# Optimization experiments

Hardware: AMD Instinct MI355X
Metric: run time of the kernel (lower is better)

The kernel has to match this reference:

```python
import jax, jax.numpy as jnp
import numpy as np

# FlowNetC correlation hyperparameters (init_kwargs)
PAD = 4            # pad_size
KERNEL = 1         # kernel_size (1x1 patch)
MD = 4             # max_displacement
STRIDE1 = 1        # stride over output positions
STRIDE2 = 1        # stride over displacements


def setup_inputs() -> dict:
    key = jax.random.key(0)
    k1, k2 = jax.random.split(key)
    input1 = jax.random.normal(k1, (8, 256, 96, 128), dtype=jnp.float32)
    input2 = jax.random.normal(k2, (8, 256, 96, 128), dtype=jnp.float32)
    return {"input1": input1, "input2": input2}


def reference(input1, input2):
    # Cost volume: out[b, d, y, x] = (1/C) * sum_c input1[b,c,y,x] * input2[b,c,y+dy,x+dx]
    # for all displacements (dy, dx) in [-MD, MD] with step STRIDE2.
    # With pad_size == max_displacement, kernel_size == 1, stride1 == 1 the output
    # spatial grid equals the input grid (FlowNetC configuration). Normalization
    # matches correlation_cuda: sumelems = kernel_size^2 * C.
    B, C, H, W = input1.shape
    p2 = jnp.pad(input2, ((0, 0), (0, 0), (PAD, PAD), (PAD, PAD)))
    disp = range(-MD, MD + 1, STRIDE2)  # 9 offsets -> 81 displacement channels
    outs = []
    for dy in disp:
        for dx in disp:
            shifted = jax.lax.dynamic_slice(p2, (0, 0, PAD + dy, PAD + dx), (B, C, H, W))
            # mean over channels == sum / (KERNEL*KERNEL*C) since KERNEL == 1
            outs.append(jnp.mean(input1 * shifted, axis=1))
    return jnp.stack(outs, axis=1)  # [B, 81, H, W]
```

## Files before the change

### kernel.cpp

```cpp
#include <hip/hip_runtime.h>
#include <hip/hip_bf16.h>


#define B_ 8
#define C_ 256
#define H_ 96
#define W_ 128
#define HW_ 12288
#define CHW_ 3145728

#define BUFSZ 40960
#define IN1_OFF 0
#define IN2_OFF 8192
#define IN2_ROWB (32 * 64)

typedef __attribute__((ext_vector_type(8))) short short8;
typedef __attribute__((ext_vector_type(4))) float f32x4;

__device__ __forceinline__ int swz16(int g, int slot) {
    return (g ^ (slot & 3) ^ ((slot >> 2) & 3)) * 16;
}

__global__ __launch_bounds__(512, 2) void corr_mfma6(
    const float* __restrict__ in1,
    const float* __restrict__ in2,
    float* __restrict__ out)
{
    __shared__ __align__(16) char lds[2 * BUFSZ];

    const int tid = threadIdx.x;

    const int blk  = blockIdx.x;
    const int b    = blk & 7;
    const int rest = blk >> 3;
    const int yt   = rest >> 3;
    const int xh   = rest & 7;

    #pragma unroll
    for (int k = 0; k < 10; ++k)
        *(f32x4*)(lds + tid * 16 + k * 8192) = f32x4{0.f, 0.f, 0.f, 0.f};

    const int lane = tid & 63;
    const int wv   = tid >> 6;
    const int ut   = wv & 1;
    const int yrh  = wv >> 1;
    const int ln   = lane & 15;
    const int qd   = lane >> 4;

    const int offA0 = IN1_OFF + ((2 * yrh) * 16 + ln) * 64 + swz16(qd, ln);
    const int pB    = 16 * ut + ln;
    const int offB  = IN2_OFF + ((2 * yrh) * 32 + pB) * 64 + swz16(qd, pB);

    const float* in1b = in1 + (size_t)b * CHW_;
    const float* in2b = in2 + (size_t)b * CHW_;

    const int pp2 = tid & 7;
    const int g2  = (tid >> 3) & 3;
    const int r2i = tid >> 5;
    const int px2 = 4 * pp2;
    const int gx2 = xh * 16 - 8 + px2;
    const int ry2 = yt * 8 - 4 + r2i;
    const bool valid2 = (gx2 >= 0) && (gx2 <= 124) && (ry2 >= 0) && (ry2 < H_);
    const int slot2 = r2i * 32 + px2;
    const float* sp2base = in2b + (size_t)(8 * g2) * HW_ + ry2 * W_ + gx2;

    const int pq1 = tid & 3;
    const int jj1 = (tid >> 2) & 3;
    const int g1  = (tid >> 4) & 3;
    const int r1i = tid >> 6;
    const int px1 = 4 * pq1;
    const int gx1 = xh * 16 + px1;
    const int y1  = yt * 8 + r1i;
    const int slot1 = r1i * 16 + px1;
    const float* sp1base = in1b + (size_t)(8 * g1 + 2 * jj1) * HW_ + y1 * W_ + gx1;

    f32x4 rA2[8], rA1[2];
    f32x4 rB2[8], rB1[2];

    auto issueA = [&](int kc) {
        const size_t ch = (size_t)kc * 32 * HW_;
        if (valid2) {
            #pragma unroll
            for (int j = 0; j < 8; ++j)
                rA2[j] = *(const f32x4*)(sp2base + ch + (size_t)j * HW_);
        }
        rA1[0] = *(const f32x4*)(sp1base + ch);
        rA1[1] = *(const f32x4*)(sp1base + ch + HW_);
    };
    auto issueB = [&](int kc) {
        const size_t ch = (size_t)kc * 32 * HW_;
        if (valid2) {
            #pragma unroll
            for (int j = 0; j < 8; ++j)
                rB2[j] = *(const f32x4*)(sp2base + ch + (size_t)j * HW_);
        }
        rB1[0] = *(const f32x4*)(sp1base + ch);
        rB1[1] = *(const f32x4*)(sp1base + ch + HW_);
    };

    auto storeA = [&](char* __restrict__ buf) {
        if (valid2) {
            #pragma unroll
            for (int p = 0; p < 4; ++p) {
                union { __hip_bfloat162 h2[4]; short8 s8; } u;
                #pragma unroll
                for (int jj = 0; jj < 4; ++jj)
                    u.h2[jj] = __float22bfloat162_rn(float2{rA2[2 * jj][p], rA2[2 * jj + 1][p]});
                *(short8*)(buf + IN2_OFF + (slot2 + p) * 64 + swz16(g2, slot2 + p)) = u.s8;
            }
        }
        #pragma unroll
        for (int p = 0; p < 4; ++p) {
            __hip_bfloat162 h = __float22bfloat162_rn(float2{rA1[0][p], rA1[1][p]});
            *(__hip_bfloat162*)(buf + IN1_OFF + (slot1 + p) * 64 + swz16(g1, slot1 + p) + 4 * jj1) = h;
        }
    };
    auto storeB = [&](char* __restrict__ buf) {
        if (valid2) {
            #pragma unroll
            for (int p = 0; p < 4; ++p) {
                union { __hip_bfloat162 h2[4]; short8 s8; } u;
                #pragma unroll
                for (int jj = 0; jj < 4; ++jj)
                    u.h2[jj] = __float22bfloat162_rn(float2{rB2[2 * jj][p], rB2[2 * jj + 1][p]});
                *(short8*)(buf + IN2_OFF + (slot2 + p) * 64 + swz16(g2, slot2 + p)) = u.s8;
            }
        }
        #pragma unroll
        for (int p = 0; p < 4; ++p) {
            __hip_bfloat162 h = __float22bfloat162_rn(float2{rB1[0][p], rB1[1][p]});
            *(__hip_bfloat162*)(buf + IN1_OFF + (slot1 + p) * 64 + swz16(g1, slot1 + p) + 4 * jj1) = h;
        }
    };

    f32x4 acc0[9], acc1[9];
    #pragma unroll
    for (int s = 0; s < 9; ++s) { acc0[s] = f32x4{0.f,0.f,0.f,0.f}; acc1[s] = f32x4{0.f,0.f,0.f,0.f}; }

    auto compute = [&](const char* __restrict__ buf) {
        short8 a0  = *(const short8*)(buf + offA0);
        short8 a1  = *(const short8*)(buf + offA0 + 16 * 64);
        short8 blo = *(const short8*)(buf + offB);
        #pragma unroll
        for (int s = 0; s < 9; ++s) {
            short8 bhi = *(const short8*)(buf + offB + (s + 1) * IN2_ROWB);
            acc0[s] = __builtin_amdgcn_mfma_f32_16x16x32_bf16(a0, blo, acc0[s], 0, 0, 0);
            acc1[s] = __builtin_amdgcn_mfma_f32_16x16x32_bf16(a1, bhi, acc1[s], 0, 0, 0);
            blo = bhi;
        }
    };

    __syncthreads();

    issueA(0);
    issueB(1);

    #pragma unroll
    for (int k2 = 0; k2 < 4; ++k2) {
        storeA(lds);
        if (2 * k2 + 2 < 8) issueA(2 * k2 + 2);
        asm volatile("s_waitcnt lgkmcnt(0)" ::: "memory");
        __builtin_amdgcn_s_barrier();
        asm volatile("" ::: "memory");
        compute(lds);
        storeB(lds + BUFSZ);
        if (2 * k2 + 3 < 8) issueB(2 * k2 + 3);
        asm volatile("s_waitcnt lgkmcnt(0)" ::: "memory");
        __builtin_amdgcn_s_barrier();
        asm volatile("" ::: "memory");
        compute(lds + BUFSZ);
    }

    __syncthreads();

    const float scale = 1.0f / 256.0f;
    float* outb = out + (size_t)b * 81 * HW_ + (size_t)(yt * 8) * W_ + xh * 16;

    #pragma unroll
    for (int s = 0; s < 9; ++s) {
        #pragma unroll
        for (int yr = 0; yr < 2; ++yr) {
            const f32x4 a = yr ? acc1[s] : acc0[s];
            const int y = 2 * yrh + yr;
            #pragma unroll
            for (int r = 0; r < 4; ++r) {
                const int m  = qd * 4 + r;
                const int dx = ln - m - 8 + 16 * ut;
                if (dx >= -4 && dx <= 4)
                    *(float*)(lds + ((y * 9 + dx + 4) * 16 + m) * 4) = a[r] * scale;
            }
        }
        asm volatile("s_waitcnt lgkmcnt(0)" ::: "memory");
        __builtin_amdgcn_s_barrier();
        asm volatile("" ::: "memory");
        #pragma unroll
        for (int i = 0; i < 3; ++i) {
            const int pidx = i * 4 + qd;
            if (pidx < 9) {
                const float v = *(const float*)(lds + ((wv * 9 + pidx) * 16 + ln) * 4);
                outb[((size_t)(s * 9 + pidx) * H_ + wv) * W_ + ln] = v;
            }
        }
        asm volatile("s_waitcnt lgkmcnt(0)" ::: "memory");
        __builtin_amdgcn_s_barrier();
        asm volatile("" ::: "memory");
    }
}

extern "C" void kernel_launch(void* const* d_in, const int* in_sizes, int n_in,
                              void* d_out, int out_size, void* d_ws, size_t ws_size,
                              hipStream_t stream) {
    const float* in1 = (const float*)d_in[0];
    const float* in2 = (const float*)d_in[1];
    float* out = (float*)d_out;

    corr_mfma6<<<768, 512, 0, stream>>>(in1, in2, out);
}
```

Measured before the change: 245.7 us.

## Split displacement rows across three blocks and unify load roles

Each block now handles only three of the nine vertical displacement rows, so the grid grows threefold and each block loads a smaller in2 halo (10 rows instead of 16). The LDS buffers shrink and launch bounds allow four blocks per CU, which raises occupancy and cuts accumulator registers. Thread roles are reorganized so some threads load in2 rows and others load in1 rows, each with full 8-channel vector loads, in place of the earlier mixed per-thread scheme. The cost is that in1 tiles and overlapping in2 halo rows are now read by three blocks instead of one, which adds global/L2 traffic.

```diff
diff --git a/kernel.cpp b/kernel.cpp
--- a/kernel.cpp
+++ b/kernel.cpp
@@ -9,7 +9,7 @@
 #define HW_ 12288
 #define CHW_ 3145728
 
-#define BUFSZ 40960
+#define BUFSZ 28672
 #define IN1_OFF 0
 #define IN2_OFF 8192
 #define IN2_ROWB (32 * 64)
@@ -21,7 +21,7 @@
     return (g ^ (slot & 3) ^ ((slot >> 2) & 3)) * 16;
 }
 
-__global__ __launch_bounds__(512, 2) void corr_mfma6(
+__global__ __launch_bounds__(512, 4) void corr_mfma8(
     const float* __restrict__ in1,
     const float* __restrict__ in2,
     float* __restrict__ out)
@@ -33,11 +33,13 @@
     const int blk  = blockIdx.x;
     const int b    = blk & 7;
     const int rest = blk >> 3;
-    const int yt   = rest >> 3;
-    const int xh   = rest & 7;
+    const int dg   = rest % 3;
+    const int t    = rest / 3;
+    const int yt   = t >> 3;
+    const int xh   = t & 7;
 
     #pragma unroll
-    for (int k = 0; k < 10; ++k)
+    for (int k = 0; k < 7; ++k)
         *(f32x4*)(lds + tid * 16 + k * 8192) = f32x4{0.f, 0.f, 0.f, 0.f};
 
     const int lane = tid & 63;
@@ -54,95 +56,71 @@
     const float* in1b = in1 + (size_t)b * CHW_;
     const float* in2b = in2 + (size_t)b * CHW_;
 
-    const int pp2 = tid & 7;
-    const int g2  = (tid >> 3) & 3;
-    const int r2i = tid >> 5;
-    const int px2 = 4 * pp2;
-    const int gx2 = xh * 16 - 8 + px2;
-    const int ry2 = yt * 8 - 4 + r2i;
-    const bool valid2 = (gx2 >= 0) && (gx2 <= 124) && (ry2 >= 0) && (ry2 < H_);
-    const int slot2 = r2i * 32 + px2;
-    const float* sp2base = in2b + (size_t)(8 * g2) * HW_ + ry2 * W_ + gx2;
+    const bool isB = tid < 320;
+    const int r_   = isB ? (tid >> 5) : ((tid - 320) >> 4);
+    const int pxq  = isB ? ((tid >> 2) & 7) : ((tid >> 2) & 3);
+    const int g_   = tid & 3;
+    const int gx   = isB ? (xh * 16 - 8 + 4 * pxq) : (xh * 16 + 4 * pxq);
+    const int gy   = isB ? (yt * 8 - 4 + 3 * dg + r_) : (yt * 8 + r_);
+    const bool vld = isB ? (gx >= 0 && gx <= 124 && gy >= 0 && gy < H_)
+                         : (tid < 448);
+    const int slot = isB ? (r_ * 32 + 4 * pxq) : (r_ * 16 + 4 * pxq);
+    const int goff = isB ? IN2_OFF : IN1_OFF;
+    const float* spbase = (isB ? in2b : in1b) + (size_t)(8 * g_) * HW_ + gy * W_ + gx;
 
-    const int pq1 = tid & 3;
-    const int jj1 = (tid >> 2) & 3;
-    const int g1  = (tid >> 4) & 3;
-    const int r1i = tid >> 6;
-    const int px1 = 4 * pq1;
-    const int gx1 = xh * 16 + px1;
-    const int y1  = yt * 8 + r1i;
-    const int slot1 = r1i * 16 + px1;
-    const float* sp1base = in1b + (size_t)(8 * g1 + 2 * jj1) * HW_ + y1 * W_ + gx1;
-
-    f32x4 rA2[8], rA1[2];
-    f32x4 rB2[8], rB1[2];
+    f32x4 rA[8], rB[8];
 
     auto issueA = [&](int kc) {
         const size_t ch = (size_t)kc * 32 * HW_;
-        if (valid2) {
+        if (vld) {
             #pragma unroll
             for (int j = 0; j < 8; ++j)
-                rA2[j] = *(const f32x4*)(sp2base + ch + (size_t)j * HW_);
+                rA[j] = *(const f32x4*)(spbase + ch + (size_t)j * HW_);
         }
-        rA1[0] = *(const f32x4*)(sp1base + ch);
-        rA1[1] = *(const f32x4*)(sp1base + ch + HW_);
     };
     auto issueB = [&](int kc) {
         const size_t ch = (size_t)kc * 32 * HW_;
-        if (valid2) {
+        if (vld) {
             #pragma unroll
             for (int j = 0; j < 8; ++j)
-                rB2[j] = *(const f32x4*)(sp2base + ch + (size_t)j * HW_);
+                rB[j] = *(const f32x4*)(spbase + ch + (size_t)j * HW_);
         }
-        rB1[0] = *(const f32x4*)(sp1base + ch);
-        rB1[1] = *(const f32x4*)(sp1base + ch + HW_);
     };
-
     auto storeA = [&](char* __restrict__ buf) {
-        if (valid2) {
+        if (vld) {
             #pragma unroll
             for (int p = 0; p < 4; ++p) {
                 union { __hip_bfloat162 h2[4]; short8 s8; } u;
                 #pragma unroll
                 for (int jj = 0; jj < 4; ++jj)
-                    u.h2[jj] = __float22bfloat162_rn(float2{rA2[2 * jj][p], rA2[2 * jj + 1][p]});
-                *(short8*)(buf + IN2_OFF + (slot2 + p) * 64 + swz16(g2, slot2 + p)) = u.s8;
+                    u.h2[jj] = __float22bfloat162_rn(float2{rA[2 * jj][p], rA[2 * jj + 1][p]});
+                *(short8*)(buf + goff + (slot + p) * 64 + swz16(g_, slot + p)) = u.s8;
             }
-        }
-        #pragma unroll
-        for (int p = 0; p < 4; ++p) {
-            __hip_bfloat162 h = __float22bfloat162_rn(float2{rA1[0][p], rA1[1][p]});
-            *(__hip_bfloat162*)(buf + IN1_OFF + (slot1 + p) * 64 + swz16(g1, slot1 + p) + 4 * jj1) = h;
         }
     };
     auto storeB = [&](char* __restrict__ buf) {
-        if (valid2) {
+        if (vld) {
             #pragma unroll
             for (int p = 0; p < 4; ++p) {
                 union { __hip_bfloat162 h2[4]; short8 s8; } u;
                 #pragma unroll
                 for (int jj = 0; jj < 4; ++jj)
-                    u.h2[jj] = __float22bfloat162_rn(float2{rB2[2 * jj][p], rB2[2 * jj + 1][p]});
-                *(short8*)(buf + IN2_OFF + (slot2 + p) * 64 + swz16(g2, slot2 + p)) = u.s8;
+                    u.h2[jj] = __float22bfloat162_rn(float2{rB[2 * jj][p], rB[2 * jj + 1][p]});
+                *(short8*)(buf + goff + (slot + p) * 64 + swz16(g_, slot + p)) = u.s8;
             }
-        }
-        #pragma unroll
-        for (int p = 0; p < 4; ++p) {
-            __hip_bfloat162 h = __float22bfloat162_rn(float2{rB1[0][p], rB1[1][p]});
-            *(__hip_bfloat162*)(buf + IN1_OFF + (slot1 + p) * 64 + swz16(g1, slot1 + p) + 4 * jj1) = h;
         }
     };
 
-    f32x4 acc0[9], acc1[9];
+    f32x4 acc0[3], acc1[3];
     #pragma unroll
-    for (int s = 0; s < 9; ++s) { acc0[s] = f32x4{0.f,0.f,0.f,0.f}; acc1[s] = f32x4{0.f,0.f,0.f,0.f}; }
+    for (int s = 0; s < 3; ++s) { acc0[s] = f32x4{0.f,0.f,0.f,0.f}; acc1[s] = f32x4{0.f,0.f,0.f,0.f}; }
 
     auto compute = [&](const char* __restrict__ buf) {
         short8 a0  = *(const short8*)(buf + offA0);
         short8 a1  = *(const short8*)(buf + offA0 + 16 * 64);
         short8 blo = *(const short8*)(buf + offB);
         #pragma unroll
-        for (int s = 0; s < 9; ++s) {
+        for (int s = 0; s < 3; ++s) {
             short8 bhi = *(const short8*)(buf + offB + (s + 1) * IN2_ROWB);
             acc0[s] = __builtin_amdgcn_mfma_f32_16x16x32_bf16(a0, blo, acc0[s], 0, 0, 0);
             acc1[s] = __builtin_amdgcn_mfma_f32_16x16x32_bf16(a1, bhi, acc1[s], 0, 0, 0);
@@ -177,7 +155,8 @@
     float* outb = out + (size_t)b * 81 * HW_ + (size_t)(yt * 8) * W_ + xh * 16;
 
     #pragma unroll
-    for (int s = 0; s < 9; ++s) {
+    for (int s = 0; s < 3; ++s) {
+        const int sf = 3 * dg + s;
         #pragma unroll
         for (int yr = 0; yr < 2; ++yr) {
             const f32x4 a = yr ? acc1[s] : acc0[s];
@@ -198,7 +177,7 @@
             const int pidx = i * 4 + qd;
             if (pidx < 9) {
                 const float v = *(const float*)(lds + ((wv * 9 + pidx) * 16 + ln) * 4);
-                outb[((size_t)(s * 9 + pidx) * H_ + wv) * W_ + ln] = v;
+                outb[((size_t)(sf * 9 + pidx) * H_ + wv) * W_ + ln] = v;
             }
         }
         asm volatile("s_waitcnt lgkmcnt(0)" ::: "memory");
@@ -214,5 +193,5 @@
     const float* in2 = (const float*)d_in[1];
     float* out = (float*)d_out;
 
-    corr_mfma6<<<768, 512, 0, stream>>>(in1, in2, out);
+    corr_mfma8<<<2304, 512, 0, stream>>>(in1, in2, out);
 }
```

Result: slower. 308.7 us (+25.6%).
